# Optimization experiments

Measured on AMD Instinct MI355X. Metric: run time of the kernel, lower is better.

The kernel has to match this reference:

```python
import jax, jax.numpy as jnp
import numpy as np

NUM_CLASSES = 5  # sleep stages: W, N1, N2, N3, REM
N = 4194304


def setup_inputs() -> dict:
    key = jax.random.key(0)
    k1, k2 = jax.random.split(key)
    inputs = jax.random.normal(k1, (N, NUM_CLASSES), dtype=jnp.float32)
    targets = jax.random.randint(k2, (N,), 0, NUM_CLASSES, dtype=jnp.int32)
    return {"inputs": inputs, "targets": targets}


def reference(inputs, targets):
    # Mean False Error loss: per-class mean of per-sample cross-entropy,
    # summed over classes that are present in the batch.
    # per-sample CE loss (stable log-softmax, single pass)
    logp = jax.nn.log_softmax(inputs, axis=-1)                    # [N, C]
    per_sample = -jnp.take_along_axis(logp, targets[:, None].astype(jnp.int32), axis=1)[:, 0]  # [N]
    # segment-reduce by class label (replaces the python grouping loop)
    loss_sums = jax.ops.segment_sum(per_sample, targets, num_segments=NUM_CLASSES)             # [C]
    counts = jax.ops.segment_sum(jnp.ones_like(per_sample), targets, num_segments=NUM_CLASSES) # [C]
    # per-class mean; empty classes contribute 0
    means = jnp.where(counts > 0, loss_sums / jnp.maximum(counts, 1.0), 0.0)
    return jnp.sum(means)
```

## Files before the change

### kernel.cpp

```cpp
#include <hip/hip_runtime.h>

#define NCLS 5
#define NSAMP 4194304
#define BLOCK 256
#define GRID 4096
#define SAMP_PER_BLOCK (NSAMP / GRID)
#define CHUNK_F4 (SAMP_PER_BLOCK * NCLS / 4)
#define NVALS (2 * NCLS)

__device__ __forceinline__ void accum_sample(float l0, float l1, float l2, float l3, float l4,
                                             int t, float sums[NCLS], unsigned int& packed_cnt) {
    float s = __expf(l0) + __expf(l1) + __expf(l2) + __expf(l3) + __expf(l4);
    float lt = (t == 0) ? l0 : (t == 1) ? l1 : (t == 2) ? l2 : (t == 3) ? l3 : l4;
    float ce = __logf(s) - lt;
#pragma unroll
    for (int k = 0; k < NCLS; ++k) {
        sums[k] += (t == k) ? ce : 0.0f;
    }
    packed_cnt += 1u << (6 * t);
}

__device__ __forceinline__ void block_reduce_10(float sums[NCLS], float cnts[NCLS],
                                                float* result10) {
#pragma unroll
    for (int k = 0; k < NCLS; ++k) {
#pragma unroll
        for (int off = 32; off > 0; off >>= 1) {
            sums[k] += __shfl_down(sums[k], off, 64);
            cnts[k] += __shfl_down(cnts[k], off, 64);
        }
    }
    __shared__ float ls[BLOCK / 64][NVALS];
    const int lane = threadIdx.x & 63;
    const int wave = threadIdx.x >> 6;
    if (lane == 0) {
#pragma unroll
        for (int k = 0; k < NCLS; ++k) {
            ls[wave][k] = sums[k];
            ls[wave][NCLS + k] = cnts[k];
        }
    }
    __syncthreads();
    if (threadIdx.x < NVALS) {
        float v = 0.f;
#pragma unroll
        for (int w = 0; w < BLOCK / 64; ++w) v += ls[w][threadIdx.x];
        *result10 = v;
    }
}

__device__ __forceinline__ int swz(int F) { return F ^ ((F >> 3) & 7); }

__device__ __forceinline__ void gload_lds16(const float4* g, float4* l) {
    __builtin_amdgcn_global_load_lds(
        (__attribute__((address_space(1))) const void*)g,
        (__attribute__((address_space(3))) void*)l, 16, 0, 0);
}

__global__ __launch_bounds__(BLOCK) void mfe_fused(const float* __restrict__ inputs,
                                                   const int* __restrict__ targets,
                                                   float* __restrict__ partial ,
                                                   unsigned int* __restrict__ flags ,
                                                   float* __restrict__ out) {
    const int T = threadIdx.x;
    const int b = blockIdx.x;
    const int w = T >> 6;
    const int lane = T & 63;
    const size_t samp0 = (size_t)b * SAMP_PER_BLOCK;
    const float4* gin = (const float4*)(inputs + samp0 * NCLS);

    __shared__ float4 lds[CHUNK_F4];

    int4 tg = *(const int4*)(targets + samp0 + 4 * T);

#pragma unroll
    for (int j = 0; j < 5; ++j) {
        const int base = 320 * w + 64 * j;
        gload_lds16(gin + swz(base + lane), &lds[base]);
    }
    asm volatile("s_waitcnt vmcnt(0)" ::: "memory");
    __syncthreads();

    float4 r[5];
#pragma unroll
    for (int k = 0; k < 5; ++k) r[k] = lds[swz(5 * T + k)];

    float sums[NCLS] = {0.f, 0.f, 0.f, 0.f, 0.f};
    unsigned int packed = 0;
    accum_sample(r[0].x, r[0].y, r[0].z, r[0].w, r[1].x, tg.x, sums, packed);
    accum_sample(r[1].y, r[1].z, r[1].w, r[2].x, r[2].y, tg.y, sums, packed);
    accum_sample(r[2].z, r[2].w, r[3].x, r[3].y, r[3].z, tg.z, sums, packed);
    accum_sample(r[3].w, r[4].x, r[4].y, r[4].z, r[4].w, tg.w, sums, packed);

    float cnts[NCLS];
#pragma unroll
    for (int k = 0; k < NCLS; ++k) {
        cnts[k] = (float)((packed >> (6 * k)) & 63u);
    }

    float total;
    block_reduce_10(sums, cnts, &total);

    if (threadIdx.x < NVALS) {
        __hip_atomic_store(&partial[threadIdx.x * GRID + blockIdx.x], total,
                           __ATOMIC_RELAXED, __HIP_MEMORY_SCOPE_AGENT);
    }
    asm volatile("s_waitcnt vmcnt(0)" ::: "memory");
    if (threadIdx.x == 0) {
        __hip_atomic_store(&flags[blockIdx.x], 1u,
                           __ATOMIC_RELAXED, __HIP_MEMORY_SCOPE_AGENT);
    }

    if (blockIdx.x != 0) return;

#pragma unroll 1
    for (int i = threadIdx.x; i < GRID; i += BLOCK) {
        while (__hip_atomic_load(&flags[i], __ATOMIC_RELAXED,
                                 __HIP_MEMORY_SCOPE_AGENT) == 0u) {
            __builtin_amdgcn_s_sleep(2);
        }
    }
    __syncthreads();
    asm volatile("" ::: "memory");

    float fsums[NCLS], fcnts[NCLS];
#pragma unroll
    for (int k = 0; k < NCLS; ++k) {
        float s = 0.f, c = 0.f;
#pragma unroll
        for (int i = 0; i < GRID / BLOCK; ++i) {
            s += __hip_atomic_load(&partial[k * GRID + threadIdx.x + i * BLOCK],
                                   __ATOMIC_RELAXED, __HIP_MEMORY_SCOPE_AGENT);
            c += __hip_atomic_load(&partial[(NCLS + k) * GRID + threadIdx.x + i * BLOCK],
                                   __ATOMIC_RELAXED, __HIP_MEMORY_SCOPE_AGENT);
        }
        fsums[k] = s;
        fcnts[k] = c;
    }

    float ftot;
    block_reduce_10(fsums, fcnts, &ftot);

    __shared__ float fin[NVALS];
    if (threadIdx.x < NVALS) fin[threadIdx.x] = ftot;
    __syncthreads();
    if (threadIdx.x == 0) {
        float loss = 0.f;
#pragma unroll
        for (int k = 0; k < NCLS; ++k) {
            float cnt = fin[NCLS + k];
            if (cnt > 0.f) loss += fin[k] / cnt;
        }
        out[0] = loss;
    }
}

extern "C" void kernel_launch(void* const* d_in, const int* in_sizes, int n_in,
                              void* d_out, int out_size, void* d_ws, size_t ws_size,
                              hipStream_t stream) {
    const float* inputs = (const float*)d_in[0];
    const int* targets = (const int*)d_in[1];
    float* out = (float*)d_out;
    float* partial = (float*)d_ws;
    unsigned int* flags =
        (unsigned int*)((char*)d_ws + (size_t)NVALS * GRID * sizeof(float));

    hipMemsetAsync(flags, 0, GRID * sizeof(unsigned int), stream);
    mfe_fused<<<GRID, BLOCK, 0, stream>>>(inputs, targets, partial, flags, out);
}
```

Before: 142.1 us.

## Halve grid and process two sample chunks per block sequentially

The grid drops from 4096 to 2048 blocks, and each block now processes two 1024-sample chunks in turn through the same LDS buffer. The reduction scratch reuses the input LDS buffer, and launch bounds request 8 blocks per CU. This halves the number of partials and flags that block 0 must poll and sum, and cuts per-block launch overhead. In exchange, the second chunk's load is serialized behind the first chunk's compute, with no double buffering, which may expose memory latency.

```diff
diff --git a/kernel.cpp b/kernel.cpp
--- a/kernel.cpp
+++ b/kernel.cpp
@@ -3,9 +3,10 @@
 #define NCLS 5
 #define NSAMP 4194304
 #define BLOCK 256
-#define GRID 4096
+#define GRID 2048
 #define SAMP_PER_BLOCK (NSAMP / GRID)
-#define CHUNK_F4 (SAMP_PER_BLOCK * NCLS / 4)
+#define CHUNK_SAMP 1024
+#define CHUNK_F4 (CHUNK_SAMP * NCLS / 4)
 #define NVALS (2 * NCLS)
 
 __device__ __forceinline__ void accum_sample(float l0, float l1, float l2, float l3, float l4,
@@ -21,7 +22,7 @@
 }
 
 __device__ __forceinline__ void block_reduce_10(float sums[NCLS], float cnts[NCLS],
-                                                float* result10) {
+                                                float* scratch, float* result10) {
 #pragma unroll
     for (int k = 0; k < NCLS; ++k) {
 #pragma unroll
@@ -30,21 +31,21 @@
             cnts[k] += __shfl_down(cnts[k], off, 64);
         }
     }
-    __shared__ float ls[BLOCK / 64][NVALS];
     const int lane = threadIdx.x & 63;
     const int wave = threadIdx.x >> 6;
+    __syncthreads();
     if (lane == 0) {
 #pragma unroll
         for (int k = 0; k < NCLS; ++k) {
-            ls[wave][k] = sums[k];
-            ls[wave][NCLS + k] = cnts[k];
+            scratch[wave * NVALS + k] = sums[k];
+            scratch[wave * NVALS + NCLS + k] = cnts[k];
         }
     }
     __syncthreads();
     if (threadIdx.x < NVALS) {
         float v = 0.f;
 #pragma unroll
-        for (int w = 0; w < BLOCK / 64; ++w) v += ls[w][threadIdx.x];
+        for (int w = 0; w < BLOCK / 64; ++w) v += scratch[w * NVALS + threadIdx.x];
         *result10 = v;
     }
 }
@@ -57,40 +58,56 @@
         (__attribute__((address_space(3))) void*)l, 16, 0, 0);
 }
 
-__global__ __launch_bounds__(BLOCK) void mfe_fused(const float* __restrict__ inputs,
-                                                   const int* __restrict__ targets,
-                                                   float* __restrict__ partial ,
-                                                   unsigned int* __restrict__ flags ,
-                                                   float* __restrict__ out) {
+__global__ __launch_bounds__(BLOCK, 8) void mfe_fused(const float* __restrict__ inputs,
+                                                      const int* __restrict__ targets,
+                                                      float* __restrict__ partial ,
+                                                      unsigned int* __restrict__ flags ,
+                                                      float* __restrict__ out) {
     const int T = threadIdx.x;
     const int b = blockIdx.x;
     const int w = T >> 6;
     const int lane = T & 63;
     const size_t samp0 = (size_t)b * SAMP_PER_BLOCK;
-    const float4* gin = (const float4*)(inputs + samp0 * NCLS);
+    const float4* gin0 = (const float4*)(inputs + samp0 * NCLS);
+    const float4* gin1 = (const float4*)(inputs + (samp0 + CHUNK_SAMP) * NCLS);
 
     __shared__ float4 lds[CHUNK_F4];
 
-    int4 tg = *(const int4*)(targets + samp0 + 4 * T);
+    int4 tg0 = *(const int4*)(targets + samp0 + 4 * T);
+    int4 tg1 = *(const int4*)(targets + samp0 + CHUNK_SAMP + 4 * T);
+
+    float sums[NCLS] = {0.f, 0.f, 0.f, 0.f, 0.f};
+    unsigned int packed = 0;
+    float4 r[5];
 
 #pragma unroll
     for (int j = 0; j < 5; ++j) {
         const int base = 320 * w + 64 * j;
-        gload_lds16(gin + swz(base + lane), &lds[base]);
+        gload_lds16(gin0 + swz(base + lane), &lds[base]);
     }
     asm volatile("s_waitcnt vmcnt(0)" ::: "memory");
     __syncthreads();
-
-    float4 r[5];
 #pragma unroll
     for (int k = 0; k < 5; ++k) r[k] = lds[swz(5 * T + k)];
+    accum_sample(r[0].x, r[0].y, r[0].z, r[0].w, r[1].x, tg0.x, sums, packed);
+    accum_sample(r[1].y, r[1].z, r[1].w, r[2].x, r[2].y, tg0.y, sums, packed);
+    accum_sample(r[2].z, r[2].w, r[3].x, r[3].y, r[3].z, tg0.z, sums, packed);
+    accum_sample(r[3].w, r[4].x, r[4].y, r[4].z, r[4].w, tg0.w, sums, packed);
+    __syncthreads();
 
-    float sums[NCLS] = {0.f, 0.f, 0.f, 0.f, 0.f};
-    unsigned int packed = 0;
-    accum_sample(r[0].x, r[0].y, r[0].z, r[0].w, r[1].x, tg.x, sums, packed);
-    accum_sample(r[1].y, r[1].z, r[1].w, r[2].x, r[2].y, tg.y, sums, packed);
-    accum_sample(r[2].z, r[2].w, r[3].x, r[3].y, r[3].z, tg.z, sums, packed);
-    accum_sample(r[3].w, r[4].x, r[4].y, r[4].z, r[4].w, tg.w, sums, packed);
+#pragma unroll
+    for (int j = 0; j < 5; ++j) {
+        const int base = 320 * w + 64 * j;
+        gload_lds16(gin1 + swz(base + lane), &lds[base]);
+    }
+    asm volatile("s_waitcnt vmcnt(0)" ::: "memory");
+    __syncthreads();
+#pragma unroll
+    for (int k = 0; k < 5; ++k) r[k] = lds[swz(5 * T + k)];
+    accum_sample(r[0].x, r[0].y, r[0].z, r[0].w, r[1].x, tg1.x, sums, packed);
+    accum_sample(r[1].y, r[1].z, r[1].w, r[2].x, r[2].y, tg1.y, sums, packed);
+    accum_sample(r[2].z, r[2].w, r[3].x, r[3].y, r[3].z, tg1.z, sums, packed);
+    accum_sample(r[3].w, r[4].x, r[4].y, r[4].z, r[4].w, tg1.w, sums, packed);
 
     float cnts[NCLS];
 #pragma unroll
@@ -98,8 +115,9 @@
         cnts[k] = (float)((packed >> (6 * k)) & 63u);
     }
 
+    float* scratch = (float*)lds;
     float total;
-    block_reduce_10(sums, cnts, &total);
+    block_reduce_10(sums, cnts, scratch, &total);
 
     if (threadIdx.x < NVALS) {
         __hip_atomic_store(&partial[threadIdx.x * GRID + blockIdx.x], total,
@@ -139,7 +157,7 @@
     }
 
     float ftot;
-    block_reduce_10(fsums, fcnts, &ftot);
+    block_reduce_10(fsums, fcnts, scratch, &ftot);
 
     __shared__ float fin[NVALS];
     if (threadIdx.x < NVALS) fin[threadIdx.x] = ftot;
```

Result: faster. 138.3 us (-2.7%).
